# Kernel optimization log

Hardware: AMD Instinct MI355X
Metric: run time of the kernel (lower is better)

The kernel has to match this reference:

```python
import jax, jax.numpy as jnp
import numpy as np

B, S, D, H = 2, 2048, 1024, 16
HD = D // H  # head_dim = 64


def setup_inputs() -> dict:
    key = jax.random.key(0)
    k1, k2, k3 = jax.random.split(key, 3)
    x = jax.random.normal(k1, (B, S, D), dtype=jnp.float32)
    W_qkv = jax.random.normal(k2, (D, 3 * D), dtype=jnp.float32) * (D ** -0.5)
    b_qkv = jnp.zeros((3 * D,), dtype=jnp.float32)
    W_proj = jax.random.normal(k3, (D, D), dtype=jnp.float32) * (D ** -0.5)
    b_proj = jnp.zeros((D,), dtype=jnp.float32)
    return {"x": x, "W_qkv": W_qkv, "b_qkv": b_qkv, "W_proj": W_proj, "b_proj": b_proj}


def reference(x, W_qkv, b_qkv, W_proj, b_proj):
    b, s, d = x.shape
    scale = HD ** -0.5
    qkv = x @ W_qkv + b_qkv                       # [B,S,3D]
    q, k, v = jnp.split(qkv, 3, axis=-1)
    # [B,S,D] -> [B,H,S,HD]
    def to_heads(t):
        return t.reshape(b, s, H, HD).transpose(0, 2, 1, 3)
    q, k, v = map(to_heads, (q, k, v))
    scores = jnp.einsum('bhqd,bhkd->bhqk', q, k) * scale  # [B,H,S,S]
    causal = jnp.triu(jnp.ones((s, s), dtype=bool), k=1)
    scores = jnp.where(causal[None, None], -jnp.inf, scores)
    attn = jax.nn.softmax(scores, axis=-1)
    out = jnp.einsum('bhqk,bhkd->bhqd', attn, v)  # [B,H,S,HD]
    out = out.transpose(0, 2, 1, 3).reshape(b, s, d)
    return out @ W_proj + b_proj
```

## Files before the change

kernel.cpp:

```cpp
#include <hip/hip_runtime.h>

using frag_t = __attribute__((ext_vector_type(8))) short;
using f32x4  = __attribute__((ext_vector_type(4))) float;

#define L2E 1.4426950408889634f

#if __has_builtin(__builtin_amdgcn_exp2f)
#define EXP2(x) __builtin_amdgcn_exp2f(x)
#else
#define EXP2(x) exp2f(x)
#endif

constexpr int B_  = 2, S_ = 2048, D_ = 1024, H_ = 16, HD_ = 64;
constexpr int M_  = B_ * S_;
constexpr float QSCALE = 0.125f * L2E;

__device__ __forceinline__ ushort f2bf(float f) {
  union { float f; unsigned u; } v; v.f = f;
  unsigned u = v.u;
  unsigned r = (u + 0x7FFFu + ((u >> 16) & 1u)) >> 16;
  return (ushort)r;
}
__device__ __forceinline__ unsigned pk_bf2(float a, float b) {
  unsigned ua = __float_as_uint(a) + 0x8000u;
  unsigned ub = __float_as_uint(b) + 0x8000u;
  return (ua >> 16) | (ub & 0xFFFF0000u);
}

__device__ __forceinline__ void gld_lds16(const ushort* g, ushort* l) {
  __builtin_amdgcn_global_load_lds((const __attribute__((address_space(1))) void*)g,
                                   (__attribute__((address_space(3))) void*)l, 16, 0, 0);
}

__global__ __launch_bounds__(256) void k_prep(
    const float* __restrict__ x, const float* __restrict__ Wqkv,
    const float* __restrict__ Wproj,
    ushort* __restrict__ Xbf, ushort* __restrict__ Wqt, ushort* __restrict__ Wpt) {
  int blk = blockIdx.x, tid = threadIdx.x;
  if (blk < 1024) {
    size_t base = (size_t)blk * 4096 + tid * 4;
    #pragma unroll
    for (int i = 0; i < 4; ++i) {
      float4 f = *(const float4*)(x + base + i * 1024);
      ushort4 o;
      o.x = f2bf(f.x); o.y = f2bf(f.y); o.z = f2bf(f.z); o.w = f2bf(f.w);
      *(ushort4*)(Xbf + base + i * 1024) = o;
    }
  } else {
    __shared__ float tile[64][65];
    const float* in; ushort* out; int N, K, bx, by;
    if (blk < 1024 + 768) { int b2 = blk - 1024; in = Wqkv;  out = Wqt; N = 3072; K = 1024; bx = b2 % 48; by = b2 / 48; }
    else                  { int b2 = blk - 1792; in = Wproj; out = Wpt; N = 1024; K = 1024; bx = b2 % 16; by = b2 / 16; }
    int n0 = bx * 64, k0 = by * 64;
    int tx = tid & 63, ty = tid >> 6;
    #pragma unroll
    for (int i = 0; i < 16; ++i)
      tile[ty + i * 4][tx] = in[(size_t)(k0 + ty + i * 4) * N + n0 + tx];
    __syncthreads();
    #pragma unroll
    for (int i = 0; i < 16; ++i)
      out[(size_t)(n0 + ty + i * 4) * K + k0 + tx] = f2bf(tile[tx][ty + i * 4]);
  }
}

__global__ __launch_bounds__(512, 2) void k_gemm8(
    const ushort* __restrict__ A, const ushort* __restrict__ Bt,
    const float* __restrict__ bias,
    ushort* __restrict__ Qo, ushort* __restrict__ Ko, ushort* __restrict__ Vo) {
  __shared__ ushort smem[65536];
  int tid = threadIdx.x;
  int lane = tid & 63, wave = tid >> 6;
  int quad = lane >> 4, li = lane & 15;
  int wm = wave >> 2, wn = wave & 3;
  int wg = blockIdx.x;
  int swz = (wg & 7) * 24 + (wg >> 3);
  int by = swz / 12, bx = swz % 12;
  int m0 = by * 256, n0 = bx * 256;
  const ushort* Asrc = A  + (size_t)m0 * 1024;
  const ushort* Bsrc = Bt + (size_t)n0 * 1024;
  int srow   = lane >> 2;
  int schunk = (lane & 3) ^ ((lane >> 4) & 3);
  int pos    = (quad ^ ((li >> 2) & 3)) * 8;

#define STG(BI, ISB, KS, KT) do { \
    const ushort* _s = (ISB) ? Bsrc : Asrc; \
    ushort* _d = &smem[((BI)*4 + (ISB)*2 + (KS)) * 8192]; \
    _Pragma("unroll") \
    for (int j = 0; j < 2; ++j) \
      gld_lds16(&_s[(size_t)(j*128 + wave*16 + srow) * 1024 + (KT)*64 + (KS)*32 + schunk*8], \
                &_d[(j*128 + wave*16) * 32]); \
  } while (0)

  f32x4 acc[8][4] = {};
  frag_t af[8], bf[2];

#define PH(BI, KS, NH, STGS, W4) do { \
    if ((NH) == 0) { \
      _Pragma("unroll") \
      for (int mi = 0; mi < 8; ++mi) \
        af[mi] = *(const frag_t*)&smem[((BI)*4 + (KS)) * 8192 + (wm*128 + mi*16 + li) * 32 + pos]; \
    } \
    _Pragma("unroll") \
    for (int nj = 0; nj < 2; ++nj) \
      bf[nj] = *(const frag_t*)&smem[((BI)*4 + 2 + (KS)) * 8192 + (wn*64 + ((NH)*2 + nj)*16 + li) * 32 + pos]; \
    STGS; \
    if (W4) asm volatile("s_waitcnt vmcnt(4)" ::: "memory"); \
    asm volatile("s_barrier" ::: "memory"); \
    __builtin_amdgcn_s_setprio(1); \
    _Pragma("unroll") \
    for (int mi = 0; mi < 8; ++mi) { \
      acc[mi][(NH)*2+0] = __builtin_amdgcn_mfma_f32_16x16x32_bf16(af[mi], bf[0], acc[mi][(NH)*2+0], 0, 0, 0); \
      acc[mi][(NH)*2+1] = __builtin_amdgcn_mfma_f32_16x16x32_bf16(af[mi], bf[1], acc[mi][(NH)*2+1], 0, 0, 0); \
    } \
    __builtin_amdgcn_s_setprio(0); \
    asm volatile("s_barrier" ::: "memory"); \
  } while (0)

  STG(0,0,0,0); STG(0,1,0,0); STG(0,0,1,0); STG(0,1,1,0);
  STG(1,0,0,1); STG(1,1,0,1);
  asm volatile("s_waitcnt vmcnt(4)" ::: "memory");
  asm volatile("s_barrier" ::: "memory");

  for (int it = 0; it < 8; ++it) {
    int t1 = 2*it + 1;
    int t2 = (2*it + 2 < 16) ? 2*it + 2 : 15;
    int t3 = (2*it + 3 < 16) ? 2*it + 3 : 15;
    PH(0,0,0, STG(1,0,1,t1), 0);
    PH(0,0,1, STG(1,1,1,t1), 0);
    PH(0,1,0, STG(0,0,0,t2), 0);
    PH(0,1,1, STG(0,1,0,t2), 1);
    PH(1,0,0, STG(0,0,1,t2), 0);
    PH(1,0,1, STG(0,1,1,t2), 0);
    PH(1,1,0, STG(1,0,0,t3), 0);
    PH(1,1,1, STG(1,1,0,t3), 1);
  }
#undef PH
#undef STG

  asm volatile("s_waitcnt vmcnt(0)" ::: "memory");
  __syncthreads();

  int which = (n0 + wn * 64) >> 10;
  if (which < 2) {
    #pragma unroll
    for (int ni = 0; ni < 4; ++ni) {
      int gcol = n0 + wn * 64 + ni * 16 + li;
      float bv = bias[gcol];
      int d = gcol & 1023, h = d >> 6, hd = d & 63;
      #pragma unroll
      for (int mi = 0; mi < 8; ++mi)
        #pragma unroll
        for (int r = 0; r < 4; ++r) {
          int grow = m0 + wm * 128 + mi * 16 + quad * 4 + r;
          int b = grow >> 11, s = grow & 2047;
          size_t off = (((size_t)b * H_ + h) * S_ + s) * HD_ + hd;
          float v = acc[mi][ni][r] + bv;
          if (which == 0) Qo[off] = f2bf(v * QSCALE);
          else            Ko[off] = f2bf(v);
        }
    }
  } else {
    ushort* vl = &smem[wave * 8192];
    #pragma unroll
    for (int ni = 0; ni < 4; ++ni) {
      int row = ni * 16 + li;
      float bv = bias[n0 + wn * 64 + row];
      int rx = (row & 7) << 3;
      #pragma unroll
      for (int mi = 0; mi < 8; ++mi)
        #pragma unroll
        for (int r = 0; r < 4; ++r) {
          int col = (mi >> 2) * 64 + quad * 16 + r * 4 + (mi & 3);
          vl[row * 128 + (col ^ rx)] = f2bf(acc[mi][ni][r] + bv);
        }
    }
    int h  = ((n0 & 1023) + wn * 64) >> 6;
    int b  = m0 >> 11;
    int s0 = (m0 & 2047) + wm * 128;
    size_t vbase = ((size_t)b * H_ + h) * HD_ * S_;
    #pragma unroll
    for (int i = 0; i < 16; ++i) {
      int row = i * 4 + quad;
      int col = li * 8;
      *(uint4*)&Vo[vbase + (size_t)row * S_ + s0 + col] =
          *(const uint4*)&vl[row * 128 + (col ^ ((row & 7) << 3))];
    }
  }
}

template <int EPI>
__global__ __launch_bounds__(256) void k_gemm(
    const ushort* __restrict__ A, const ushort* __restrict__ Bt,
    const float* __restrict__ bias,
    ushort* __restrict__ Qo, ushort* __restrict__ Ko, ushort* __restrict__ Vo,
    float* __restrict__ Co, int N, int K) {
  constexpr int BM = (EPI == 0) ? 128 : 64;
  constexpr int BN = 64, BK = 64;
  constexpr int MI = (EPI == 0) ? 4 : 2, NI = 2;
  __shared__ ushort smem[(BM + BN) * BK];
  ushort* As = smem;
  ushort* Bs = smem + BM * BK;
  int tid  = threadIdx.x;
  int lane = tid & 63, wave = tid >> 6;
  int quad = lane >> 4, li = lane & 15;
  int mbase = (wave >> 1) * (MI * 16);
  int nbase = (wave & 1) * 32;
  int m0 = blockIdx.y * BM, n0 = blockIdx.x * BN;
  int srow = lane >> 3;
  int scol = ((lane & 7) ^ srow) * 8;
  f32x4 acc[MI][NI] = {};
  for (int k0 = 0; k0 < K; k0 += BK) {
    if (EPI == 0) {
      #pragma unroll
      for (int i = 0; i < 4; ++i) {
        int rbase = i * 32 + wave * 8;
        gld_lds16(&A[(size_t)(m0 + rbase + srow) * K + k0 + scol], &As[rbase * BK]);
      }
    } else {
      #pragma unroll
      for (int i = 0; i < 2; ++i) {
        int rbase = wave * 16 + i * 8;
        gld_lds16(&A[(size_t)(m0 + rbase + srow) * K + k0 + scol], &As[rbase * BK]);
      }
    }
    #pragma unroll
    for (int i = 0; i < 2; ++i) {
      int rbase = wave * 16 + i * 8;
      gld_lds16(&Bt[(size_t)(n0 + rbase + srow) * K + k0 + scol], &Bs[rbase * BK]);
    }
    __syncthreads();
    #pragma unroll
    for (int ks = 0; ks < 2; ++ks) {
      frag_t af[MI], bf[NI];
      #pragma unroll
      for (int mi = 0; mi < MI; ++mi)
        af[mi] = *(const frag_t*)&As[(mbase + mi * 16 + li) * BK + (((ks * 4 + quad) ^ (li & 7)) * 8)];
      #pragma unroll
      for (int ni = 0; ni < NI; ++ni)
        bf[ni] = *(const frag_t*)&Bs[(nbase + ni * 16 + li) * BK + (((ks * 4 + quad) ^ (li & 7)) * 8)];
      #pragma unroll
      for (int mi = 0; mi < MI; ++mi)
        #pragma unroll
        for (int ni = 0; ni < NI; ++ni)
          acc[mi][ni] = __builtin_amdgcn_mfma_f32_16x16x32_bf16(af[mi], bf[ni], acc[mi][ni], 0, 0, 0);
    }
    __syncthreads();
  }
  if (EPI == 1) {
    #pragma unroll
    for (int mi = 0; mi < MI; ++mi)
      #pragma unroll
      for (int ni = 0; ni < NI; ++ni) {
        int gcol = n0 + nbase + ni * 16 + li;
        float bv = bias[gcol];
        #pragma unroll
        for (int r = 0; r < 4; ++r) {
          int grow = m0 + mbase + mi * 16 + quad * 4 + r;
          Co[(size_t)grow * N + gcol] = acc[mi][ni][r] + bv;
        }
      }
  }
}

__global__ __launch_bounds__(256) void k_attn(
    const ushort* __restrict__ Q, const ushort* __restrict__ K,
    const ushort* __restrict__ Vt, ushort* __restrict__ O) {
  __shared__ ushort Kbuf[2][64 * 64];
  __shared__ ushort Vbuf[2][64 * 64];
  __shared__ ushort Plds[4 * 16 * 64];
  int lane = threadIdx.x & 63, wave = threadIdx.x >> 6;
  int quad = lane >> 4, li = lane & 15;
  int bh = blockIdx.x;
  int qb = 31 - (int)blockIdx.y;
  int b = bh >> 4, h = bh & 15;
  int q0 = qb * 64 + wave * 16;
  const ushort* Qb = Q  + (size_t)bh * S_ * HD_;
  const ushort* Kb = K  + (size_t)bh * S_ * HD_;
  const ushort* Vb = Vt + (size_t)bh * HD_ * S_;
  ushort* Pw = &Plds[wave * 1024];

  frag_t qf[2];
  #pragma unroll
  for (int ks = 0; ks < 2; ++ks)
    qf[ks] = *(const frag_t*)&Qb[(size_t)(q0 + li) * HD_ + ks * 32 + quad * 8];

  frag_t ones;
  #pragma unroll
  for (int i = 0; i < 8; ++i) ones[i] = (short)0x3F80;

  f32x4 o[4] = {};
  f32x4 lacc = {};

  auto stage = [&](int kb, int bi) {
    #pragma unroll
    for (int i = 0; i < 2; ++i) {
      int rt  = wave * 16 + i * 8 + (lane >> 3);
      int c16 = (lane & 7) ^ (lane >> 3);
      gld_lds16(&Kb[(size_t)(kb * 64 + rt) * HD_ + c16 * 8], &Kbuf[bi][(wave * 16 + i * 8) * 64]);
      gld_lds16(&Vb[(size_t)rt * S_ + kb * 64 + c16 * 8],    &Vbuf[bi][(wave * 16 + i * 8) * 64]);
    }
  };

  auto comp = [&](int kb, bool diag, int bi) {
    f32x4 sc[4];
    #pragma unroll
    for (int t = 0; t < 4; ++t) {
      f32x4 a = {};
      #pragma unroll
      for (int ks = 0; ks < 2; ++ks) {
        frag_t kf = *(const frag_t*)&Kbuf[bi][(t * 16 + li) * 64 + (((quad + ks * 4) ^ (li & 7)) * 8)];
        a = __builtin_amdgcn_mfma_f32_16x16x32_bf16(qf[ks], kf, a, 0, 0, 0);
      }
      sc[t] = a;
    }
    if (diag) {
      #pragma unroll
      for (int t = 0; t < 4; ++t) {
        int key = kb * 64 + t * 16 + li;
        #pragma unroll
        for (int r = 0; r < 4; ++r)
          if (key > q0 + quad * 4 + r) sc[t][r] = -1e30f;
      }
    }
    #pragma unroll
    for (int t = 0; t < 4; ++t)
      #pragma unroll
      for (int r = 0; r < 4; ++r)
        sc[t][r] = EXP2(sc[t][r]);
    #pragma unroll
    for (int r = 0; r < 4; ++r) {
      int row = quad * 4 + r;
      uint2 w;
      w.x = pk_bf2(sc[0][r], sc[1][r]);
      w.y = pk_bf2(sc[2][r], sc[3][r]);
      *(uint2*)&Pw[row * 64 + ((li ^ (row & 6)) * 4)] = w;
    }
    frag_t pf[2];
    #pragma unroll
    for (int ks = 0; ks < 2; ++ks) {
      int g0 = (ks * 4 + quad) * 2;
      pf[ks] = *(const frag_t*)&Pw[li * 64 + ((g0 ^ (li & 6)) * 4)];
    }
    lacc = __builtin_amdgcn_mfma_f32_16x16x32_bf16(pf[0], ones, lacc, 0, 0, 0);
    lacc = __builtin_amdgcn_mfma_f32_16x16x32_bf16(pf[1], ones, lacc, 0, 0, 0);
    #pragma unroll
    for (int t = 0; t < 4; ++t)
      #pragma unroll
      for (int ks = 0; ks < 2; ++ks) {
        frag_t vf = *(const frag_t*)&Vbuf[bi][(t * 16 + li) * 64 + (((quad + ks * 4) ^ (li & 7)) * 8)];
        o[t] = __builtin_amdgcn_mfma_f32_16x16x32_bf16(pf[ks], vf, o[t], 0, 0, 0);
      }
  };

  stage(0, 0);
  __syncthreads();
  for (int kb = 0; kb <= qb; ++kb) {
    if (kb < qb) stage(kb + 1, (kb + 1) & 1);
    comp(kb, kb == qb, kb & 1);
    __syncthreads();
  }

  #pragma unroll
  for (int r = 0; r < 4; ++r) {
    float inv = 1.f / lacc[r];
    int srow = q0 + quad * 4 + r;
    #pragma unroll
    for (int ht = 0; ht < 4; ++ht)
      O[((size_t)b * S_ + srow) * D_ + h * 64 + ht * 16 + li] = f2bf(o[ht][r] * inv);
  }
}

extern "C" void kernel_launch(void* const* d_in, const int* in_sizes, int n_in,
                              void* d_out, int out_size, void* d_ws, size_t ws_size,
                              hipStream_t stream) {
  (void)in_sizes; (void)n_in; (void)out_size; (void)ws_size;
  const float* x     = (const float*)d_in[0];
  const float* Wqkv  = (const float*)d_in[1];
  const float* bqkv  = (const float*)d_in[2];
  const float* Wproj = (const float*)d_in[3];
  const float* bproj = (const float*)d_in[4];
  float* out = (float*)d_out;

  char* ws = (char*)d_ws;
  ushort* Xbf = (ushort*)(ws);
  ushort* Wqt = (ushort*)(ws + (8u  << 20));
  ushort* Wpt = (ushort*)(ws + (14u << 20));
  ushort* Qbf = (ushort*)(ws + (16u << 20));
  ushort* Kbf = (ushort*)(ws + (24u << 20));
  ushort* Vtb = (ushort*)(ws + (32u << 20));
  ushort* Obf = Xbf;

  k_prep<<<dim3(2048), dim3(256), 0, stream>>>(x, Wqkv, Wproj, Xbf, Wqt, Wpt);
  k_gemm8<<<dim3(192), dim3(512), 0, stream>>>(Xbf, Wqt, bqkv, Qbf, Kbf, Vtb);
  k_attn<<<dim3(B_ * H_, 32), dim3(256), 0, stream>>>(Qbf, Kbf, Vtb, Obf);
  k_gemm<1><<<dim3(16, 64), dim3(256), 0, stream>>>(Obf, Wpt, bproj,
                                                    (ushort*)nullptr, (ushort*)nullptr, (ushort*)nullptr,
                                                    out, D_, D_);
}
```

Measured before the change: 170.1 us.

## Give each attention wave 32 query rows to reuse K/V fragments

Each attention workgroup now covers 128 query rows, with each wave owning two 16-row query tiles. Every K and V fragment read from shared memory therefore feeds two MFMAs, which halves the K/V staging traffic per query and halves the grid. Waves skip key blocks that lie entirely past their causal limit. The cost is more registers per wave, fewer blocks (512) to balance causal work across, and some idle waves near the diagonal. The gemm template also loses its unused QKV-epilogue parameters as cleanup.

New measurement: 187.1 us. 10.0% more time.

```diff
diff --git a/kernel.cpp b/kernel.cpp
--- a/kernel.cpp
+++ b/kernel.cpp
@@ -192,11 +192,10 @@
 __global__ __launch_bounds__(256) void k_gemm(
     const ushort* __restrict__ A, const ushort* __restrict__ Bt,
     const float* __restrict__ bias,
-    ushort* __restrict__ Qo, ushort* __restrict__ Ko, ushort* __restrict__ Vo,
     float* __restrict__ Co, int N, int K) {
-  constexpr int BM = (EPI == 0) ? 128 : 64;
+  constexpr int BM = 64;
   constexpr int BN = 64, BK = 64;
-  constexpr int MI = (EPI == 0) ? 4 : 2, NI = 2;
+  constexpr int MI = 2, NI = 2;
   __shared__ ushort smem[(BM + BN) * BK];
   ushort* As = smem;
   ushort* Bs = smem + BM * BK;
@@ -210,18 +209,10 @@
   int scol = ((lane & 7) ^ srow) * 8;
   f32x4 acc[MI][NI] = {};
   for (int k0 = 0; k0 < K; k0 += BK) {
-    if (EPI == 0) {
-      #pragma unroll
-      for (int i = 0; i < 4; ++i) {
-        int rbase = i * 32 + wave * 8;
-        gld_lds16(&A[(size_t)(m0 + rbase + srow) * K + k0 + scol], &As[rbase * BK]);
-      }
-    } else {
-      #pragma unroll
-      for (int i = 0; i < 2; ++i) {
-        int rbase = wave * 16 + i * 8;
-        gld_lds16(&A[(size_t)(m0 + rbase + srow) * K + k0 + scol], &As[rbase * BK]);
-      }
+    #pragma unroll
+    for (int i = 0; i < 2; ++i) {
+      int rbase = wave * 16 + i * 8;
+      gld_lds16(&A[(size_t)(m0 + rbase + srow) * K + k0 + scol], &As[rbase * BK]);
     }
     #pragma unroll
     for (int i = 0; i < 2; ++i) {
@@ -246,20 +237,18 @@
     }
     __syncthreads();
   }
-  if (EPI == 1) {
-    #pragma unroll
-    for (int mi = 0; mi < MI; ++mi)
-      #pragma unroll
-      for (int ni = 0; ni < NI; ++ni) {
-        int gcol = n0 + nbase + ni * 16 + li;
-        float bv = bias[gcol];
-        #pragma unroll
-        for (int r = 0; r < 4; ++r) {
-          int grow = m0 + mbase + mi * 16 + quad * 4 + r;
-          Co[(size_t)grow * N + gcol] = acc[mi][ni][r] + bv;
-        }
+  #pragma unroll
+  for (int mi = 0; mi < MI; ++mi)
+    #pragma unroll
+    for (int ni = 0; ni < NI; ++ni) {
+      int gcol = n0 + nbase + ni * 16 + li;
+      float bv = bias[gcol];
+      #pragma unroll
+      for (int r = 0; r < 4; ++r) {
+        int grow = m0 + mbase + mi * 16 + quad * 4 + r;
+        Co[(size_t)grow * N + gcol] = acc[mi][ni][r] + bv;
       }
-  }
+    }
 }
 
 __global__ __launch_bounds__(256) void k_attn(
@@ -267,29 +256,31 @@
     const ushort* __restrict__ Vt, ushort* __restrict__ O) {
   __shared__ ushort Kbuf[2][64 * 64];
   __shared__ ushort Vbuf[2][64 * 64];
-  __shared__ ushort Plds[4 * 16 * 64];
+  __shared__ ushort Plds[4 * 32 * 64];
   int lane = threadIdx.x & 63, wave = threadIdx.x >> 6;
   int quad = lane >> 4, li = lane & 15;
   int bh = blockIdx.x;
-  int qb = 31 - (int)blockIdx.y;
-  int b = bh >> 4, h = bh & 15;
-  int q0 = qb * 64 + wave * 16;
+  int qt = 15 - (int)blockIdx.y;
+  int b = bh >> 4, hh = bh & 15;
+  int q0 = qt * 128 + wave * 32;
   const ushort* Qb = Q  + (size_t)bh * S_ * HD_;
   const ushort* Kb = K  + (size_t)bh * S_ * HD_;
   const ushort* Vb = Vt + (size_t)bh * HD_ * S_;
-  ushort* Pw = &Plds[wave * 1024];
-
-  frag_t qf[2];
+  ushort* Pw = &Plds[wave * 2048];
+
+  frag_t qf[2][2];
   #pragma unroll
-  for (int ks = 0; ks < 2; ++ks)
-    qf[ks] = *(const frag_t*)&Qb[(size_t)(q0 + li) * HD_ + ks * 32 + quad * 8];
+  for (int h = 0; h < 2; ++h)
+    #pragma unroll
+    for (int ks = 0; ks < 2; ++ks)
+      qf[h][ks] = *(const frag_t*)&Qb[(size_t)(q0 + h * 16 + li) * HD_ + ks * 32 + quad * 8];
 
   frag_t ones;
   #pragma unroll
   for (int i = 0; i < 8; ++i) ones[i] = (short)0x3F80;
 
-  f32x4 o[4] = {};
-  f32x4 lacc = {};
+  f32x4 o[2][4] = {};
+  f32x4 lacc[2] = {};
 
   auto stage = [&](int kb, int bi) {
     #pragma unroll
@@ -302,72 +293,91 @@
   };
 
   auto comp = [&](int kb, bool diag, int bi) {
-    f32x4 sc[4];
+    f32x4 sc[2][4];
     #pragma unroll
     for (int t = 0; t < 4; ++t) {
-      f32x4 a = {};
+      frag_t kf0 = *(const frag_t*)&Kbuf[bi][(t * 16 + li) * 64 + ((quad ^ (li & 7)) * 8)];
+      frag_t kf1 = *(const frag_t*)&Kbuf[bi][(t * 16 + li) * 64 + (((quad + 4) ^ (li & 7)) * 8)];
+      #pragma unroll
+      for (int h = 0; h < 2; ++h) {
+        f32x4 a = {};
+        a = __builtin_amdgcn_mfma_f32_16x16x32_bf16(qf[h][0], kf0, a, 0, 0, 0);
+        a = __builtin_amdgcn_mfma_f32_16x16x32_bf16(qf[h][1], kf1, a, 0, 0, 0);
+        sc[h][t] = a;
+      }
+    }
+    if (diag) {
+      #pragma unroll
+      for (int h = 0; h < 2; ++h)
+        #pragma unroll
+        for (int t = 0; t < 4; ++t) {
+          int key = kb * 64 + t * 16 + li;
+          #pragma unroll
+          for (int r = 0; r < 4; ++r)
+            if (key > q0 + h * 16 + quad * 4 + r) sc[h][t][r] = -1e30f;
+        }
+    }
+    #pragma unroll
+    for (int h = 0; h < 2; ++h)
+      #pragma unroll
+      for (int t = 0; t < 4; ++t)
+        #pragma unroll
+        for (int r = 0; r < 4; ++r)
+          sc[h][t][r] = EXP2(sc[h][t][r]);
+    #pragma unroll
+    for (int h = 0; h < 2; ++h)
+      #pragma unroll
+      for (int r = 0; r < 4; ++r) {
+        int row = quad * 4 + r;
+        uint2 w;
+        w.x = pk_bf2(sc[h][0][r], sc[h][1][r]);
+        w.y = pk_bf2(sc[h][2][r], sc[h][3][r]);
+        *(uint2*)&Pw[(h * 16 + row) * 64 + ((li ^ (row & 6)) * 4)] = w;
+      }
+    frag_t pf[2][2];
+    #pragma unroll
+    for (int h = 0; h < 2; ++h)
       #pragma unroll
       for (int ks = 0; ks < 2; ++ks) {
-        frag_t kf = *(const frag_t*)&Kbuf[bi][(t * 16 + li) * 64 + (((quad + ks * 4) ^ (li & 7)) * 8)];
-        a = __builtin_amdgcn_mfma_f32_16x16x32_bf16(qf[ks], kf, a, 0, 0, 0);
+        int g0 = (ks * 4 + quad) * 2;
+        pf[h][ks] = *(const frag_t*)&Pw[(h * 16 + li) * 64 + ((g0 ^ (li & 6)) * 4)];
       }
-      sc[t] = a;
-    }
-    if (diag) {
-      #pragma unroll
-      for (int t = 0; t < 4; ++t) {
-        int key = kb * 64 + t * 16 + li;
-        #pragma unroll
-        for (int r = 0; r < 4; ++r)
-          if (key > q0 + quad * 4 + r) sc[t][r] = -1e30f;
-      }
-    }
-    #pragma unroll
-    for (int t = 0; t < 4; ++t)
-      #pragma unroll
-      for (int r = 0; r < 4; ++r)
-        sc[t][r] = EXP2(sc[t][r]);
-    #pragma unroll
-    for (int r = 0; r < 4; ++r) {
-      int row = quad * 4 + r;
-      uint2 w;
-      w.x = pk_bf2(sc[0][r], sc[1][r]);
-      w.y = pk_bf2(sc[2][r], sc[3][r]);
-      *(uint2*)&Pw[row * 64 + ((li ^ (row & 6)) * 4)] = w;
-    }
-    frag_t pf[2];
-    #pragma unroll
-    for (int ks = 0; ks < 2; ++ks) {
-      int g0 = (ks * 4 + quad) * 2;
-      pf[ks] = *(const frag_t*)&Pw[li * 64 + ((g0 ^ (li & 6)) * 4)];
-    }
-    lacc = __builtin_amdgcn_mfma_f32_16x16x32_bf16(pf[0], ones, lacc, 0, 0, 0);
-    lacc = __builtin_amdgcn_mfma_f32_16x16x32_bf16(pf[1], ones, lacc, 0, 0, 0);
+    #pragma unroll
+    for (int h = 0; h < 2; ++h) {
+      lacc[h] = __builtin_amdgcn_mfma_f32_16x16x32_bf16(pf[h][0], ones, lacc[h], 0, 0, 0);
+      lacc[h] = __builtin_amdgcn_mfma_f32_16x16x32_bf16(pf[h][1], ones, lacc[h], 0, 0, 0);
+    }
     #pragma unroll
     for (int t = 0; t < 4; ++t)
       #pragma unroll
       for (int ks = 0; ks < 2; ++ks) {
         frag_t vf = *(const frag_t*)&Vbuf[bi][(t * 16 + li) * 64 + (((quad + ks * 4) ^ (li & 7)) * 8)];
-        o[t] = __builtin_amdgcn_mfma_f32_16x16x32_bf16(pf[ks], vf, o[t], 0, 0, 0);
+        #pragma unroll
+        for (int h = 0; h < 2; ++h)
+          o[h][t] = __builtin_amdgcn_mfma_f32_16x16x32_bf16(pf[h][ks], vf, o[h][t], 0, 0, 0);
       }
   };
 
   stage(0, 0);
   __syncthreads();
-  for (int kb = 0; kb <= qb; ++kb) {
-    if (kb < qb) stage(kb + 1, (kb + 1) & 1);
-    comp(kb, kb == qb, kb & 1);
+  int kmax = 2 * qt + 1;
+  for (int kb = 0; kb <= kmax; ++kb) {
+    if (kb < kmax) stage(kb + 1, (kb + 1) & 1);
+    if (kb * 64 <= q0 + 31)
+      comp(kb, kb * 64 + 63 > q0, kb & 1);
     __syncthreads();
   }
 
   #pragma unroll
-  for (int r = 0; r < 4; ++r) {
-    float inv = 1.f / lacc[r];
-    int srow = q0 + quad * 4 + r;
-    #pragma unroll
-    for (int ht = 0; ht < 4; ++ht)
-      O[((size_t)b * S_ + srow) * D_ + h * 64 + ht * 16 + li] = f2bf(o[ht][r] * inv);
-  }
+  for (int h = 0; h < 2; ++h)
+    #pragma unroll
+    for (int r = 0; r < 4; ++r) {
+      float inv = 1.f / lacc[h][r];
+      int srow = q0 + h * 16 + quad * 4 + r;
+      #pragma unroll
+      for (int ht = 0; ht < 4; ++ht)
+        O[((size_t)b * S_ + srow) * D_ + hh * 64 + ht * 16 + li] = f2bf(o[h][ht][r] * inv);
+    }
 }
 
 extern "C" void kernel_launch(void* const* d_in, const int* in_sizes, int n_in,
@@ -392,8 +402,6 @@
 
   k_prep<<<dim3(2048), dim3(256), 0, stream>>>(x, Wqkv, Wproj, Xbf, Wqt, Wpt);
   k_gemm8<<<dim3(192), dim3(512), 0, stream>>>(Xbf, Wqt, bqkv, Qbf, Kbf, Vtb);
-  k_attn<<<dim3(B_ * H_, 32), dim3(256), 0, stream>>>(Qbf, Kbf, Vtb, Obf);
-  k_gemm<1><<<dim3(16, 64), dim3(256), 0, stream>>>(Obf, Wpt, bproj,
-                                                    (ushort*)nullptr, (ushort*)nullptr, (ushort*)nullptr,
-                                                    out, D_, D_);
-}
+  k_attn<<<dim3(B_ * H_, 16), dim3(256), 0, stream>>>(Qbf, Kbf, Vtb, Obf);
+  k_gemm<1><<<dim3(16, 64), dim3(256), 0, stream>>>(Obf, Wpt, bproj, out, D_, D_);
+}
```

## Keep attention probabilities in registers via transposed MFMA and permlane swap

Applied to the files above, without the earlier changes.

The attention kernel now computes S^T by swapping the MFMA operands, so each lane holds scores for one query. Probabilities are packed to bf16 with v_cvt_pk_bf16_f32 and redistributed with v_permlane32_swap instead of a round trip through LDS. The V tile layout written by the QKV GEMM epilogue is permuted to match the new fragment ordering, and the output store becomes packed 8-byte writes. This removes the LDS write and read of P per block and its latency. In exchange it relies on inline asm for gfx950 instructions and couples the V layout tightly to the register permutation. Unused GEMM template code is also removed.

New measurement: 169.4 us. About the same (-0.4%).

```diff
diff --git a/kernel.cpp b/kernel.cpp
--- a/kernel.cpp
+++ b/kernel.cpp
@@ -20,11 +20,6 @@
   unsigned u = v.u;
   unsigned r = (u + 0x7FFFu + ((u >> 16) & 1u)) >> 16;
   return (ushort)r;
-}
-__device__ __forceinline__ unsigned pk_bf2(float a, float b) {
-  unsigned ua = __float_as_uint(a) + 0x8000u;
-  unsigned ub = __float_as_uint(b) + 0x8000u;
-  return (ua >> 16) | (ub & 0xFFFF0000u);
 }
 
 __device__ __forceinline__ void gld_lds16(const ushort* g, ushort* l) {
@@ -167,12 +162,16 @@
       float bv = bias[n0 + wn * 64 + row];
       int rx = (row & 7) << 3;
       #pragma unroll
-      for (int mi = 0; mi < 8; ++mi)
+      for (int mi = 0; mi < 8; ++mi) {
+        int g  = (mi & 1) * 4 + quad;
+        int gm = g & 3;
+        int gp = (gm == 1 || gm == 2) ? (g ^ 3) : g;
         #pragma unroll
         for (int r = 0; r < 4; ++r) {
-          int col = (mi >> 2) * 64 + quad * 16 + r * 4 + (mi & 3);
+          int col = (mi >> 1) * 32 + gp * 4 + r;
           vl[row * 128 + (col ^ rx)] = f2bf(acc[mi][ni][r] + bv);
         }
+      }
     }
     int h  = ((n0 & 1023) + wn * 64) >> 6;
     int b  = m0 >> 11;
@@ -192,11 +191,10 @@
 __global__ __launch_bounds__(256) void k_gemm(
     const ushort* __restrict__ A, const ushort* __restrict__ Bt,
     const float* __restrict__ bias,
-    ushort* __restrict__ Qo, ushort* __restrict__ Ko, ushort* __restrict__ Vo,
     float* __restrict__ Co, int N, int K) {
-  constexpr int BM = (EPI == 0) ? 128 : 64;
+  constexpr int BM = 64;
   constexpr int BN = 64, BK = 64;
-  constexpr int MI = (EPI == 0) ? 4 : 2, NI = 2;
+  constexpr int MI = 2, NI = 2;
   __shared__ ushort smem[(BM + BN) * BK];
   ushort* As = smem;
   ushort* Bs = smem + BM * BK;
@@ -210,18 +208,10 @@
   int scol = ((lane & 7) ^ srow) * 8;
   f32x4 acc[MI][NI] = {};
   for (int k0 = 0; k0 < K; k0 += BK) {
-    if (EPI == 0) {
-      #pragma unroll
-      for (int i = 0; i < 4; ++i) {
-        int rbase = i * 32 + wave * 8;
-        gld_lds16(&A[(size_t)(m0 + rbase + srow) * K + k0 + scol], &As[rbase * BK]);
-      }
-    } else {
-      #pragma unroll
-      for (int i = 0; i < 2; ++i) {
-        int rbase = wave * 16 + i * 8;
-        gld_lds16(&A[(size_t)(m0 + rbase + srow) * K + k0 + scol], &As[rbase * BK]);
-      }
+    #pragma unroll
+    for (int i = 0; i < 2; ++i) {
+      int rbase = wave * 16 + i * 8;
+      gld_lds16(&A[(size_t)(m0 + rbase + srow) * K + k0 + scol], &As[rbase * BK]);
     }
     #pragma unroll
     for (int i = 0; i < 2; ++i) {
@@ -246,20 +236,18 @@
     }
     __syncthreads();
   }
-  if (EPI == 1) {
-    #pragma unroll
-    for (int mi = 0; mi < MI; ++mi)
-      #pragma unroll
-      for (int ni = 0; ni < NI; ++ni) {
-        int gcol = n0 + nbase + ni * 16 + li;
-        float bv = bias[gcol];
-        #pragma unroll
-        for (int r = 0; r < 4; ++r) {
-          int grow = m0 + mbase + mi * 16 + quad * 4 + r;
-          Co[(size_t)grow * N + gcol] = acc[mi][ni][r] + bv;
-        }
-      }
-  }
+  #pragma unroll
+  for (int mi = 0; mi < MI; ++mi)
+    #pragma unroll
+    for (int ni = 0; ni < NI; ++ni) {
+      int gcol = n0 + nbase + ni * 16 + li;
+      float bv = bias[gcol];
+      #pragma unroll
+      for (int r = 0; r < 4; ++r) {
+        int grow = m0 + mbase + mi * 16 + quad * 4 + r;
+        Co[(size_t)grow * N + gcol] = acc[mi][ni][r] + bv;
+      }
+    }
 }
 
 __global__ __launch_bounds__(256) void k_attn(
@@ -267,17 +255,15 @@
     const ushort* __restrict__ Vt, ushort* __restrict__ O) {
   __shared__ ushort Kbuf[2][64 * 64];
   __shared__ ushort Vbuf[2][64 * 64];
-  __shared__ ushort Plds[4 * 16 * 64];
   int lane = threadIdx.x & 63, wave = threadIdx.x >> 6;
   int quad = lane >> 4, li = lane & 15;
   int bh = blockIdx.x;
   int qb = 31 - (int)blockIdx.y;
-  int b = bh >> 4, h = bh & 15;
+  int b = bh >> 4, hh = bh & 15;
   int q0 = qb * 64 + wave * 16;
   const ushort* Qb = Q  + (size_t)bh * S_ * HD_;
   const ushort* Kb = K  + (size_t)bh * S_ * HD_;
   const ushort* Vb = Vt + (size_t)bh * HD_ * S_;
-  ushort* Pw = &Plds[wave * 1024];
 
   frag_t qf[2];
   #pragma unroll
@@ -309,17 +295,17 @@
       #pragma unroll
       for (int ks = 0; ks < 2; ++ks) {
         frag_t kf = *(const frag_t*)&Kbuf[bi][(t * 16 + li) * 64 + (((quad + ks * 4) ^ (li & 7)) * 8)];
-        a = __builtin_amdgcn_mfma_f32_16x16x32_bf16(qf[ks], kf, a, 0, 0, 0);
+        a = __builtin_amdgcn_mfma_f32_16x16x32_bf16(kf, qf[ks], a, 0, 0, 0);
       }
       sc[t] = a;
     }
     if (diag) {
       #pragma unroll
       for (int t = 0; t < 4; ++t) {
-        int key = kb * 64 + t * 16 + li;
+        int key = kb * 64 + t * 16 + quad * 4;
         #pragma unroll
         for (int r = 0; r < 4; ++r)
-          if (key > q0 + quad * 4 + r) sc[t][r] = -1e30f;
+          if (key + r > q0 + li) sc[t][r] = -1e30f;
       }
     }
     #pragma unroll
@@ -327,28 +313,29 @@
       #pragma unroll
       for (int r = 0; r < 4; ++r)
         sc[t][r] = EXP2(sc[t][r]);
-    #pragma unroll
-    for (int r = 0; r < 4; ++r) {
-      int row = quad * 4 + r;
-      uint2 w;
-      w.x = pk_bf2(sc[0][r], sc[1][r]);
-      w.y = pk_bf2(sc[2][r], sc[3][r]);
-      *(uint2*)&Pw[row * 64 + ((li ^ (row & 6)) * 4)] = w;
-    }
+
     frag_t pf[2];
     #pragma unroll
     for (int ks = 0; ks < 2; ++ks) {
-      int g0 = (ks * 4 + quad) * 2;
-      pf[ks] = *(const frag_t*)&Pw[li * 64 + ((g0 ^ (li & 6)) * 4)];
-    }
-    lacc = __builtin_amdgcn_mfma_f32_16x16x32_bf16(pf[0], ones, lacc, 0, 0, 0);
-    lacc = __builtin_amdgcn_mfma_f32_16x16x32_bf16(pf[1], ones, lacc, 0, 0, 0);
-    #pragma unroll
-    for (int t = 0; t < 4; ++t)
+      unsigned w0e, w1e, w0o, w1o;
+      asm("v_cvt_pk_bf16_f32 %0, %1, %2" : "=v"(w0e) : "v"(sc[2*ks][0]),   "v"(sc[2*ks][1]));
+      asm("v_cvt_pk_bf16_f32 %0, %1, %2" : "=v"(w1e) : "v"(sc[2*ks][2]),   "v"(sc[2*ks][3]));
+      asm("v_cvt_pk_bf16_f32 %0, %1, %2" : "=v"(w0o) : "v"(sc[2*ks+1][0]), "v"(sc[2*ks+1][1]));
+      asm("v_cvt_pk_bf16_f32 %0, %1, %2" : "=v"(w1o) : "v"(sc[2*ks+1][2]), "v"(sc[2*ks+1][3]));
+      asm("v_permlane32_swap_b32 %0, %1" : "+v"(w0e), "+v"(w0o));
+      asm("v_permlane32_swap_b32 %0, %1" : "+v"(w1e), "+v"(w1o));
+      union { frag_t f; unsigned u[4]; } pu;
+      pu.u[0] = w0e; pu.u[1] = w1e; pu.u[2] = w0o; pu.u[3] = w1o;
+      pf[ks] = pu.f;
+    }
+    lacc = __builtin_amdgcn_mfma_f32_16x16x32_bf16(ones, pf[0], lacc, 0, 0, 0);
+    lacc = __builtin_amdgcn_mfma_f32_16x16x32_bf16(ones, pf[1], lacc, 0, 0, 0);
+    #pragma unroll
+    for (int ht = 0; ht < 4; ++ht)
       #pragma unroll
       for (int ks = 0; ks < 2; ++ks) {
-        frag_t vf = *(const frag_t*)&Vbuf[bi][(t * 16 + li) * 64 + (((quad + ks * 4) ^ (li & 7)) * 8)];
-        o[t] = __builtin_amdgcn_mfma_f32_16x16x32_bf16(pf[ks], vf, o[t], 0, 0, 0);
+        frag_t vtf = *(const frag_t*)&Vbuf[bi][(ht * 16 + li) * 64 + (((ks * 4 + quad) ^ (li & 7)) * 8)];
+        o[ht] = __builtin_amdgcn_mfma_f32_16x16x32_bf16(vtf, pf[ks], o[ht], 0, 0, 0);
       }
   };
 
@@ -360,13 +347,16 @@
     __syncthreads();
   }
 
+  float inv = 1.f / lacc[0];
+  int srow = q0 + li;
+  size_t obase = ((size_t)b * S_ + srow) * D_ + hh * 64 + quad * 4;
   #pragma unroll
-  for (int r = 0; r < 4; ++r) {
-    float inv = 1.f / lacc[r];
-    int srow = q0 + quad * 4 + r;
-    #pragma unroll
-    for (int ht = 0; ht < 4; ++ht)
-      O[((size_t)b * S_ + srow) * D_ + h * 64 + ht * 16 + li] = f2bf(o[ht][r] * inv);
+  for (int ht = 0; ht < 4; ++ht) {
+    unsigned lo, hi;
+    asm("v_cvt_pk_bf16_f32 %0, %1, %2" : "=v"(lo) : "v"(o[ht][0] * inv), "v"(o[ht][1] * inv));
+    asm("v_cvt_pk_bf16_f32 %0, %1, %2" : "=v"(hi) : "v"(o[ht][2] * inv), "v"(o[ht][3] * inv));
+    uint2 w; w.x = lo; w.y = hi;
+    *(uint2*)&O[obase + ht * 16] = w;
   }
 }
 
@@ -393,7 +383,5 @@
   k_prep<<<dim3(2048), dim3(256), 0, stream>>>(x, Wqkv, Wproj, Xbf, Wqt, Wpt);
   k_gemm8<<<dim3(192), dim3(512), 0, stream>>>(Xbf, Wqt, bqkv, Qbf, Kbf, Vtb);
   k_attn<<<dim3(B_ * H_, 32), dim3(256), 0, stream>>>(Qbf, Kbf, Vtb, Obf);
-  k_gemm<1><<<dim3(16, 64), dim3(256), 0, stream>>>(Obf, Wpt, bproj,
-                                                    (ushort*)nullptr, (ushort*)nullptr, (ushort*)nullptr,
-                                                    out, D_, D_);
-}
+  k_gemm<1><<<dim3(16, 64), dim3(256), 0, stream>>>(Obf, Wpt, bproj, out, D_, D_);
+}
```
